# Performance work log

Measured on AMD Instinct MI355X. Metric: run time of the kernel, lower is better.

## Reference

```python
import jax, jax.numpy as jnp
import numpy as np

EPS = 1e-5

def conv3x3(x, w, b=None):
    # NCHW, OIHW, stride 1, padding 1
    y = jax.lax.conv_general_dilated(x, w, (1, 1), ((1, 1), (1, 1)),
                                     dimension_numbers=('NCHW', 'OIHW', 'NCHW'))
    if b is not None:
        y = y + b[None, :, None, None]
    return y

def batchnorm(x, g, b):
    # training-mode BN (PyTorch default): biased variance over (N,H,W)
    m = x.mean((0, 2, 3), keepdims=True)
    v = x.var((0, 2, 3), keepdims=True)
    return (x - m) * jax.lax.rsqrt(v + EPS) * g[None, :, None, None] + b[None, :, None, None]

def upsample2x_align_corners(x):
    # bilinear, align_corners=True, scale_factor=2
    def lerp_axis(a, Lin, axis):
        Lout = 2 * Lin
        c = jnp.arange(Lout, dtype=a.dtype) * (Lin - 1) / (Lout - 1)
        i0 = jnp.floor(c).astype(jnp.int32)
        i1 = jnp.minimum(i0 + 1, Lin - 1)
        w = c - i0.astype(a.dtype)
        shape = [1] * a.ndim
        shape[axis] = Lout
        w = w.reshape(shape)
        return jnp.take(a, i0, axis=axis) * (1 - w) + jnp.take(a, i1, axis=axis) * w
    x = lerp_axis(x, x.shape[2], 2)
    x = lerp_axis(x, x.shape[3], 3)
    return x

def deform_sample(x, offsets):
    # torchvision DeformConv2d v1 sampling: kernel 3x3, pad 1, offsets [B,18,H,W]
    # layout: per kernel point k (row-major), channels (2k, 2k+1) = (dy, dx)
    B, C, H, W = x.shape
    K = 9
    off = offsets.reshape(B, K, 2, H, W)
    ky, kx = jnp.meshgrid(jnp.arange(3) - 1, jnp.arange(3) - 1, indexing='ij')
    ky = ky.reshape(K).astype(x.dtype)
    kx = kx.reshape(K).astype(x.dtype)
    gy = jnp.arange(H, dtype=x.dtype)[None, None, :, None]
    gx = jnp.arange(W, dtype=x.dtype)[None, None, None, :]
    py = gy + ky[None, :, None, None] + off[:, :, 0]  # [B,K,H,W]
    px = gx + kx[None, :, None, None] + off[:, :, 1]
    y0 = jnp.floor(py)
    x0 = jnp.floor(px)
    wy = (py - y0)[:, None]  # [B,1,K,H,W]
    wx = (px - x0)[:, None]
    y0i = y0.astype(jnp.int32)
    x0i = x0.astype(jnp.int32)
    x_flat = x.reshape(B, C, H * W)
    def gather(yi, xi):
        valid = ((yi >= 0) & (yi < H) & (xi >= 0) & (xi < W))
        idx = jnp.clip(yi, 0, H - 1) * W + jnp.clip(xi, 0, W - 1)  # [B,K,H,W]
        g = jnp.take_along_axis(x_flat, idx.reshape(B, 1, K * H * W), axis=2)
        return g.reshape(B, C, K, H, W) * valid[:, None].astype(x.dtype)
    v00 = gather(y0i, x0i)
    v01 = gather(y0i, x0i + 1)
    v10 = gather(y0i + 1, x0i)
    v11 = gather(y0i + 1, x0i + 1)
    return (v00 * (1 - wy) * (1 - wx) + v01 * (1 - wy) * wx
            + v10 * wy * (1 - wx) + v11 * wy * wx)

def setup_inputs() -> dict:
    key = jax.random.key(0)
    ks = jax.random.split(key, 6)
    B, in_ch, skip_ch, out_ch = 4, 256, 128, 128
    Hs, Ws = 128, 128
    x = jax.random.normal(ks[0], (B, in_ch, Hs // 2, Ws // 2), jnp.float32)
    skip = jax.random.normal(ks[1], (B, skip_ch, Hs, Ws), jnp.float32)
    cat_ch = in_ch + skip_ch
    conv1_w = jax.random.normal(ks[2], (out_ch, cat_ch, 3, 3), jnp.float32) * (2.0 / (cat_ch * 9)) ** 0.5
    off_w = jax.random.normal(ks[3], (18, out_ch, 3, 3), jnp.float32) * 0.01
    off_b = jnp.zeros((18,), jnp.float32)
    def_w = jax.random.normal(ks[4], (out_ch, out_ch, 3, 3), jnp.float32) * (2.0 / (out_ch * 9)) ** 0.5
    def_b = jnp.zeros((out_ch,), jnp.float32)
    return {
        'x': x, 'skip': skip,
        'conv1_w': conv1_w,
        'bn1_g': jnp.ones((out_ch,), jnp.float32), 'bn1_b': jnp.zeros((out_ch,), jnp.float32),
        'off_w': off_w, 'off_b': off_b,
        'def_w': def_w, 'def_b': def_b,
        'bn2_g': jnp.ones((out_ch,), jnp.float32), 'bn2_b': jnp.zeros((out_ch,), jnp.float32),
    }

def reference(x, skip, conv1_w, bn1_g, bn1_b, off_w, off_b, def_w, def_b, bn2_g, bn2_b):
    xu = upsample2x_align_corners(x)
    dh = skip.shape[2] - xu.shape[2]
    dw = skip.shape[3] - xu.shape[3]
    if dh != 0 or dw != 0:
        xu = jnp.pad(xu, ((0, 0), (0, 0), (dh // 2, dh - dh // 2), (dw // 2, dw - dw // 2)))
    cat = jnp.concatenate([skip, xu], axis=1)
    h = jax.nn.relu(batchnorm(conv3x3(cat, conv1_w), bn1_g, bn1_b))
    offsets = conv3x3(h, off_w, off_b)  # [B,18,H,W]
    sampled = deform_sample(h, offsets)  # [B,C,9,H,W]
    O = def_w.shape[0]
    y = jnp.einsum('ock,bckhw->bohw', def_w.reshape(O, def_w.shape[1], 9), sampled)
    y = y + def_b[None, :, None, None]
    return jax.nn.relu(batchnorm(y, bn2_g, bn2_b))
```

## Files before the change

kernel.cpp:

```cpp
#include <hip/hip_runtime.h>
#include <hip/hip_bf16.h>

typedef __hip_bfloat16 bf16;
typedef __bf16 bf16x8 __attribute__((ext_vector_type(8)));
typedef __bf16 bf16x4 __attribute__((ext_vector_type(4)));
typedef float  f32x4  __attribute__((ext_vector_type(4)));

constexpr int NB   = 4;
constexpr int H    = 128;
constexpr int W    = 128;
constexpr int HW   = H * W;
constexpr int NPIX = NB * HW;
constexpr int CCAT = 384;
constexpr int CSKIP= 128;
constexpr int CIN  = 256;
constexpr int CO   = 128;
constexpr int HS   = 64;
constexpr int WP   = 130;
constexpr int K1   = 3456;
constexpr int KD   = 1152;
constexpr int NBORD= 2 * WP + 2 * (WP - 2);
constexpr float EPS = 1e-5f;

__device__ __forceinline__ float b2f(bf16 v){ return __bfloat162float(v); }
__device__ __forceinline__ bf16  f2b(float v){ return __float2bfloat16(v); }

__device__ __forceinline__ void async_copy16(const void* g, void* s){
    __builtin_amdgcn_global_load_lds((const __attribute__((address_space(1))) void*)g,
                                     (__attribute__((address_space(3))) void*)s, 16, 0, 0);
}

__device__ __forceinline__ void border_yx(int p, int& y, int& x){
    if (p < WP)             { y = 0;        x = p; }
    else if (p < 2 * WP)    { y = WP - 1;   x = p - WP; }
    else if (p < 2 * WP + (WP - 2)) { y = p - 2 * WP + 1;          x = 0; }
    else                    { y = p - (2 * WP + (WP - 2)) + 1;     x = WP - 1; }
}

__global__ void k_prep(float* __restrict__ sums, bf16* __restrict__ catp,
                       bf16* __restrict__ hp){
    int i = blockIdx.x * blockDim.x + threadIdx.x;
    int stride = gridDim.x * blockDim.x;
    for (int j = i; j < 512; j += stride) sums[j] = 0.f;
    const int nCat = NB * NBORD * CCAT;
    for (int j = i; j < nCat; j += stride){
        int c = j % CCAT, r = j / CCAT, p = r % NBORD, b = r / NBORD;
        int y, x; border_yx(p, y, x);
        catp[(((size_t)b * WP + y) * WP + x) * CCAT + c] = f2b(0.f);
    }
    const int nHp = NB * NBORD * CO;
    for (int j = i; j < nHp; j += stride){
        int c = j % CO, r = j / CO, p = r % NBORD, b = r / NBORD;
        int y, x; border_yx(p, y, x);
        hp[(((size_t)b * WP + y) * WP + x) * CO + c] = f2b(0.f);
    }
}

__global__ __launch_bounds__(256) void k_build_cat2(const float* __restrict__ x,
                                                    const float* __restrict__ skip,
                                                    bf16* __restrict__ catp){
    constexpr int TS = 66;
    __shared__ bf16 tile[128 * TS];
    int t  = threadIdx.x;
    int y  = blockIdx.x % H, b = blockIdx.x / H;
    int xx = t & 127, cp = t >> 7;

    float cy = (y * 63.0f) / 127.0f;
    int   y0 = (int)cy;
    int   y1 = min(y0 + 1, HS - 1);
    float wy = cy - y0;
    float cxf = (xx * 63.0f) / 127.0f;
    int   x0 = (int)cxf;
    int   x1 = min(x0 + 1, HS - 1);
    float wx = cxf - x0;

    bf16* orow = catp + (((size_t)b * WP + y + 1) * WP + 1) * CCAT;

    for (int chunk = 0; chunk < 6; chunk++){
        int cbase = chunk * 64;
        if (chunk >= 1) __syncthreads();
        if (chunk < 2){
            const float* sb = skip + ((size_t)(b * CSKIP + cbase + cp * 32) * H + y) * W;
#pragma unroll
            for (int i = 0; i < 32; i++)
                tile[xx * TS + cp * 32 + i] = f2b(sb[(size_t)i * HW + xx]);
        } else {
            int icb = (chunk - 2) * 64 + cp * 32;
            const float* xr0 = x + ((size_t)(b * CIN + icb) * HS + y0) * HS;
            const float* xr1 = x + ((size_t)(b * CIN + icb) * HS + y1) * HS;
#pragma unroll
            for (int i = 0; i < 32; i++){
                const float* r0 = xr0 + (size_t)i * HS * HS;
                const float* r1 = xr1 + (size_t)i * HS * HS;
                float v0 = r0[x0] * (1 - wx) + r0[x1] * wx;
                float v1 = r1[x0] * (1 - wx) + r1[x1] * wx;
                tile[xx * TS + cp * 32 + i] = f2b(v0 * (1 - wy) + v1 * wy);
            }
        }
        __syncthreads();
        int cc2 = (t & 31) * 2;
        int px0 = t >> 5;
#pragma unroll
        for (int pp = 0; pp < 16; pp++){
            int px = pp * 8 + px0;
            unsigned int v = *(const unsigned int*)&tile[px * TS + cc2];
            *(unsigned int*)&orow[(size_t)px * CCAT + cbase + cc2] = v;
        }
    }
}

__global__ void k_tr_all(const float* __restrict__ w1, const float* __restrict__ wo,
                         const float* __restrict__ wd,
                         bf16* __restrict__ wt1, bf16* __restrict__ wto,
                         bf16* __restrict__ wtd){
    int i = blockIdx.x * blockDim.x + threadIdx.x;
    if (i < CO * K1){
        int k = i % K1, oc = i / K1;
        int ky = k / 1152, r = k % 1152, kx = r / 384, ic = r % 384;
        wt1[i] = f2b(w1[((oc * CCAT + ic) * 3 + ky) * 3 + kx]);
        return;
    }
    i -= CO * K1;
    if (i < 32 * KD){
        int kk = i % KD, o = i / KD;
        int ky = kk / 384, r = kk % 384, kx = r >> 7, ic = r & 127;
        wto[i] = (o < 18) ? f2b(wo[((o * CO + ic) * 3 + ky) * 3 + kx]) : f2b(0.f);
        return;
    }
    i -= 32 * KD;
    if (i < CO * KD){
        int kk = i % KD, o = i / KD;
        int kp = kk >> 7, c = kk & 127;
        wtd[i] = f2b(wd[(o * CO + c) * 9 + kp]);
    }
}

__global__ __launch_bounds__(256) void k_conv1_mfma(const bf16* __restrict__ catp,
                                                    const bf16* __restrict__ wbt,
                                                    bf16* __restrict__ hp,
                                                    float* __restrict__ sums){
    __shared__ unsigned short Ab[132 * 128];
    __shared__ unsigned short Bb[128 * 64];
    __shared__ float ps[256];
    int t = threadIdx.x;
    int l = t & 63, w = t >> 6;
    int y = blockIdx.x % H, b = blockIdx.x / H;

    int pr   = l >> 3;
    int koct = (l & 7) ^ pr;
    int m    = l & 15, quad = l >> 4;
    int wm   = w & 1,  wn   = w >> 1;

    f32x4 acc[4][4];
#pragma unroll
    for (int i = 0; i < 4; i++)
#pragma unroll
        for (int j = 0; j < 4; j++) acc[i][j] = f32x4{0.f, 0.f, 0.f, 0.f};

    const size_t rowStride = (size_t)WP * CCAT;
    for (int ky = 0; ky < 3; ky++){
        const bf16* Arow = catp + ((size_t)(b * WP) + y + ky) * rowStride;
        for (int ci = 0; ci < 3; ci++){
            __syncthreads();
            for (int i = w; i < 33; i += 4){
                int G  = i * 64 + l;
                int px = G >> 4, ol = G & 15;
                int osrc = ol ^ (px & 7);
                async_copy16(Arow + (size_t)px * CCAT + ci * 128 + osrc * 8,
                             &Ab[i * 512]);
            }
            for (int kx = 0; kx < 3; kx++){
                for (int s64 = 0; s64 < 2; s64++){
                    if (kx | s64) __syncthreads();
                    int kg = ky * 1152 + kx * 384 + ci * 128 + s64 * 64;
#pragma unroll
                    for (int i = 0; i < 4; i++){
                        int ocg = w * 32 + i * 8;
                        async_copy16(wbt + (size_t)(ocg + pr) * K1 + kg + koct * 8,
                                     &Bb[ocg * 64]);
                    }
                    __syncthreads();
                    const bf16x8* ap = (const bf16x8*)Ab;
                    const bf16x8* bp = (const bf16x8*)Bb;
#pragma unroll
                    for (int ks = 0; ks < 2; ks++){
                        int s = s64 * 2 + ks;
                        bf16x8 af[4], bfr[4];
#pragma unroll
                        for (int mi = 0; mi < 4; mi++){
                            int pxk = wm * 64 + mi * 16 + m + kx;
                            af[mi] = ap[pxk * 16 + ((s * 4 + quad) ^ (pxk & 7))];
                        }
#pragma unroll
                        for (int ni = 0; ni < 4; ni++){
                            int oc = wn * 64 + ni * 16 + m;
                            bfr[ni] = bp[oc * 8 + ((ks * 4 + quad) ^ (oc & 7))];
                        }
#pragma unroll
                        for (int mi = 0; mi < 4; mi++)
#pragma unroll
                            for (int ni = 0; ni < 4; ni++)
                                acc[mi][ni] = __builtin_amdgcn_mfma_f32_16x16x32_bf16(
                                    af[mi], bfr[ni], acc[mi][ni], 0, 0, 0);
                    }
                }
            }
        }
    }
    size_t obase = (((size_t)b * WP + y + 1) * WP + 1) * CO;
#pragma unroll
    for (int mi = 0; mi < 4; mi++){
        int p0 = wm * 64 + mi * 16 + quad * 4;
#pragma unroll
        for (int ni = 0; ni < 4; ni++){
            int oc = wn * 64 + ni * 16 + m;
#pragma unroll
            for (int r = 0; r < 4; r++)
                hp[obase + (size_t)(p0 + r) * CO + oc] = f2b(acc[mi][ni][r]);
        }
    }
    ps[t] = 0.f;
    __syncthreads();
#pragma unroll
    for (int ni = 0; ni < 4; ni++){
        int ch = wn * 64 + ni * 16 + m;
        float s = 0.f, q = 0.f;
#pragma unroll
        for (int mi = 0; mi < 4; mi++)
#pragma unroll
            for (int r = 0; r < 4; r++){
                float v = acc[mi][ni][r];
                s += v; q += v * v;
            }
        s += __shfl_xor(s, 16); s += __shfl_xor(s, 32);
        q += __shfl_xor(q, 16); q += __shfl_xor(q, 32);
        if (quad == 0){
            atomicAdd(&ps[ch], s);
            atomicAdd(&ps[128 + ch], q);
        }
    }
    __syncthreads();
    if (t < 128){
        atomicAdd(&sums[t],       ps[t]);
        atomicAdd(&sums[128 + t], ps[128 + t]);
    }
}

__global__ __launch_bounds__(256) void k_bn_apply_pad(bf16* __restrict__ t,
                                                      const float* __restrict__ sums,
                                                      const float* __restrict__ g,
                                                      const float* __restrict__ bb){
    __shared__ float ssc[256];
    int tt = threadIdx.x;
    if (tt < 128){
        float mean = sums[tt] / (float)NPIX;
        float var  = sums[128 + tt] / (float)NPIX - mean * mean;
        float scale = g[tt] * rsqrtf(var + EPS);
        ssc[tt]       = scale;
        ssc[128 + tt] = bb[tt] - mean * scale;
    }
    __syncthreads();
    int i = blockIdx.x * 256 + tt;
    if (i >= NPIX * CO) return;
    int c = i & 127;
    int pix = i >> 7;
    int xw = pix & 127, yh = (pix >> 7) & 127, b = pix >> 14;
    size_t a = (((size_t)b * WP + yh + 1) * WP + xw + 1) * CO + c;
    float v = b2f(t[a]) * ssc[c] + ssc[128 + c];
    t[a] = f2b(v > 0.f ? v : 0.f);
}

__global__ __launch_bounds__(256) void k_conv_off_mfma(const bf16* __restrict__ hp,
                                                       const bf16* __restrict__ wob,
                                                       const float* __restrict__ off_b,
                                                       bf16* __restrict__ offs){
    __shared__ unsigned short Ab[132 * 128];
    __shared__ unsigned short Bb[32 * 384];
    int t = threadIdx.x, l = t & 63, w = t >> 6;
    int y = blockIdx.x % H, b = blockIdx.x / H;
    int m = l & 15, quad = l >> 4;
    int wm = w & 1, wn = w >> 1;

    f32x4 acc[4];
#pragma unroll
    for (int i = 0; i < 4; i++) acc[i] = f32x4{0.f, 0.f, 0.f, 0.f};

    const size_t rowStrideH = (size_t)WP * CO;
    for (int ky = 0; ky < 3; ky++){
        const bf16* Arow = hp + ((size_t)(b * WP) + y + ky) * rowStrideH;
        __syncthreads();
        for (int i = w; i < 33; i += 4){
            int G  = i * 64 + l;
            int px = G >> 4, ol = G & 15;
            int osrc = ol ^ (px & 7);
            async_copy16(Arow + (size_t)px * CO + osrc * 8, &Ab[i * 512]);
        }
        for (int i = w; i < 24; i += 4){
            int g  = i * 64 + l;
            int kx = g >> 9, oc = (g >> 4) & 31, ol = g & 15;
            int osrc = ol ^ (oc & 7);
            async_copy16(wob + (size_t)oc * KD + ky * 384 + kx * 128 + osrc * 8,
                         &Bb[i * 512]);
        }
        __syncthreads();
        const bf16x8* ap = (const bf16x8*)Ab;
        const bf16x8* bp = (const bf16x8*)Bb;
        for (int kx = 0; kx < 3; kx++){
#pragma unroll
            for (int s = 0; s < 4; s++){
                int oc = wn * 16 + m;
                bf16x8 bfr = bp[kx * 512 + oc * 16 + ((s * 4 + quad) ^ (oc & 7))];
#pragma unroll
                for (int mi = 0; mi < 4; mi++){
                    int pxk = wm * 64 + mi * 16 + m + kx;
                    bf16x8 af = ap[pxk * 16 + ((s * 4 + quad) ^ (pxk & 7))];
                    acc[mi] = __builtin_amdgcn_mfma_f32_16x16x32_bf16(af, bfr, acc[mi], 0, 0, 0);
                }
            }
        }
    }
    int oc = wn * 16 + m;
    if (oc < 18){
        float bias = off_b[oc];
        int rowpix = b * HW + y * W;
#pragma unroll
        for (int mi = 0; mi < 4; mi++){
            int p0 = wm * 64 + mi * 16 + quad * 4;
#pragma unroll
            for (int r = 0; r < 4; r++)
                offs[(size_t)(rowpix + p0 + r) * 18 + oc] = f2b(acc[mi][r] + bias);
        }
    }
}

__global__ __launch_bounds__(256) void k_deform_mfma(const bf16* __restrict__ hp,
                                                     const bf16* __restrict__ offs,
                                                     const bf16* __restrict__ wdb,
                                                     const float* __restrict__ def_b,
                                                     bf16* __restrict__ y,
                                                     float* __restrict__ sums){
    __shared__ unsigned short Ab[128 * 64];
    __shared__ unsigned short Bb[128 * 64];
    __shared__ int2   sc_yx[9 * 128];
    __shared__ float4 sc_w[9 * 128];
    __shared__ float  ps[256];

    int t = threadIdx.x, l = t & 63, w = t >> 6;
    int yrow = blockIdx.x % H, b = blockIdx.x / H;
    int rowpix = b * HW + yrow * W;

    for (int idx = t; idx < 9 * 128; idx += 256){
        int kp = idx >> 7, px = idx & 127;
        float dy = b2f(offs[(size_t)(rowpix + px) * 18 + 2 * kp]);
        float dx = b2f(offs[(size_t)(rowpix + px) * 18 + 2 * kp + 1]);
        float py = yrow + (kp / 3 - 1) + dy;
        float pxx = px + (kp % 3 - 1) + dx;
        float fy = floorf(py), fx = floorf(pxx);
        float wy = py - fy, wx = pxx - fx;
        int y0 = (int)fy, x0 = (int)fx;
        bool vy0 = (y0 >= 0) && (y0 < H);
        bool vy1 = (y0 + 1 >= 0) && (y0 + 1 < H);
        bool vx0 = (x0 >= 0) && (x0 < W);
        bool vx1 = (x0 + 1 >= 0) && (x0 + 1 < W);
        int y0c = min(max(y0, 0), H - 1),     y1c = min(max(y0 + 1, 0), H - 1);
        int x0c = min(max(x0, 0), W - 1),     x1c = min(max(x0 + 1, 0), W - 1);
        sc_yx[idx] = make_int2(((y0c + 1) * WP) | (((y1c + 1) * WP) << 16),
                               (x0c + 1) | ((x1c + 1) << 16));
        sc_w[idx] = make_float4((1 - wy) * (1 - wx) * (float)(vy0 && vx0),
                                (1 - wy) * wx       * (float)(vy0 && vx1),
                                wy * (1 - wx)       * (float)(vy1 && vx0),
                                wy * wx             * (float)(vy1 && vx1));
    }
    __syncthreads();

    int pr = l >> 3, koct = (l & 7) ^ pr;
    int m = l & 15, quad = l >> 4;
    int wm = w & 1, wn = w >> 1;
    int g = l >> 4, j = l & 15;

    f32x4 acc[4][4];
#pragma unroll
    for (int i = 0; i < 4; i++)
#pragma unroll
        for (int jj = 0; jj < 4; jj++) acc[i][jj] = f32x4{0.f, 0.f, 0.f, 0.f};

    const bf16* hpb = hp + (size_t)b * WP * WP * CO;

    for (int kc = 0; kc < 18; kc++){
        int kp = kc >> 1, ch = (kc & 1) * 64;
        __syncthreads();
        int kg = kp * 128 + ch;
#pragma unroll
        for (int i = 0; i < 4; i++){
            int oc = w * 32 + i * 8 + pr;
            async_copy16(wdb + (size_t)oc * KD + kg + koct * 8,
                         &Bb[(w * 32 + i * 8) * 64]);
        }
        int cb = ch + j * 4;
#pragma unroll
        for (int p = 0; p < 8; p++){
            int px = w * 32 + g * 8 + p;
            int idx = kp * 128 + px;
            int2 yx = sc_yx[idx];
            float4 w4 = sc_w[idx];
            int r0 = yx.x & 0xffff, r1 = ((unsigned)yx.x) >> 16;
            int c0 = yx.y & 0xffff, c1 = ((unsigned)yx.y) >> 16;
            const bf16* base = hpb + cb;
            bf16x4 s00 = *(const bf16x4*)(base + (size_t)(r0 + c0) * CO);
            bf16x4 s01 = *(const bf16x4*)(base + (size_t)(r0 + c1) * CO);
            bf16x4 s10 = *(const bf16x4*)(base + (size_t)(r1 + c0) * CO);
            bf16x4 s11 = *(const bf16x4*)(base + (size_t)(r1 + c1) * CO);
            bf16x4 pv;
#pragma unroll
            for (int r = 0; r < 4; r++){
                float v = w4.x * (float)s00[r] + w4.y * (float)s01[r]
                        + w4.z * (float)s10[r] + w4.w * (float)s11[r];
                pv[r] = (__bf16)v;
            }
            int oct_sw = (j >> 1) ^ (px & 7);
            *(bf16x4*)&Ab[px * 64 + oct_sw * 8 + (j & 1) * 4] = pv;
        }
        __syncthreads();
        const bf16x8* ap = (const bf16x8*)Ab;
        const bf16x8* bp = (const bf16x8*)Bb;
#pragma unroll
        for (int ks = 0; ks < 2; ks++){
            bf16x8 af[4], bfr[4];
#pragma unroll
            for (int mi = 0; mi < 4; mi++){
                int px = wm * 64 + mi * 16 + m;
                af[mi] = ap[px * 8 + ((ks * 4 + quad) ^ (px & 7))];
            }
#pragma unroll
            for (int ni = 0; ni < 4; ni++){
                int oc = wn * 64 + ni * 16 + m;
                bfr[ni] = bp[oc * 8 + ((ks * 4 + quad) ^ (oc & 7))];
            }
#pragma unroll
            for (int mi = 0; mi < 4; mi++)
#pragma unroll
                for (int ni = 0; ni < 4; ni++)
                    acc[mi][ni] = __builtin_amdgcn_mfma_f32_16x16x32_bf16(
                        af[mi], bfr[ni], acc[mi][ni], 0, 0, 0);
        }
    }
#pragma unroll
    for (int mi = 0; mi < 4; mi++){
        int p0 = wm * 64 + mi * 16 + quad * 4;
#pragma unroll
        for (int ni = 0; ni < 4; ni++){
            int oc = wn * 64 + ni * 16 + m;
            float bias = def_b[oc];
#pragma unroll
            for (int r = 0; r < 4; r++)
                y[(size_t)(rowpix + p0 + r) * CO + oc] = f2b(acc[mi][ni][r] + bias);
        }
    }
    ps[t] = 0.f;
    __syncthreads();
#pragma unroll
    for (int ni = 0; ni < 4; ni++){
        int ch = wn * 64 + ni * 16 + m;
        float bias = def_b[ch];
        float s = 0.f, q = 0.f;
#pragma unroll
        for (int mi = 0; mi < 4; mi++)
#pragma unroll
            for (int r = 0; r < 4; r++){
                float v = acc[mi][ni][r] + bias;
                s += v; q += v * v;
            }
        s += __shfl_xor(s, 16); s += __shfl_xor(s, 32);
        q += __shfl_xor(q, 16); q += __shfl_xor(q, 32);
        if (quad == 0){
            atomicAdd(&ps[ch], s);
            atomicAdd(&ps[128 + ch], q);
        }
    }
    __syncthreads();
    if (t < 128){
        atomicAdd(&sums[t],       ps[t]);
        atomicAdd(&sums[128 + t], ps[128 + t]);
    }
}

__global__ __launch_bounds__(256) void k_final(const bf16* __restrict__ yb,
                                               const float* __restrict__ sums,
                                               const float* __restrict__ g,
                                               const float* __restrict__ bb,
                                               float* __restrict__ out){
    __shared__ unsigned short tile[128 * 129];
    __shared__ float ssc[256];
    int t = threadIdx.x;
    if (t < 128){
        float mean = sums[t] / (float)NPIX;
        float var  = sums[128 + t] / (float)NPIX - mean * mean;
        float scale = g[t] * rsqrtf(var + EPS);
        ssc[t]       = scale;
        ssc[128 + t] = bb[t] - mean * scale;
    }
    int yrow = blockIdx.x % H, b = blockIdx.x / H;
    int rowbase = b * HW + yrow * W;
    const unsigned short* src = (const unsigned short*)yb;
    for (int it = 0; it < 64; it++){
        int idx = it * 256 + t;
        int c = idx & 127, px = idx >> 7;
        tile[px * 129 + c] = src[(size_t)(rowbase + px) * CO + c];
    }
    __syncthreads();
    for (int it = 0; it < 64; it++){
        int idx = it * 256 + t;
        int xw = idx & 127, o = idx >> 7;
        unsigned short u = tile[xw * 129 + o];
        float v = (float)(*(const __bf16*)&u);
        v = v * ssc[o] + ssc[128 + o];
        out[(((size_t)b * CO + o) * H + yrow) * W + xw] = v > 0.f ? v : 0.f;
    }
}

extern "C" void kernel_launch(void* const* d_in, const int* in_sizes, int n_in,
                              void* d_out, int out_size, void* d_ws, size_t ws_size,
                              hipStream_t stream){
    const float* x      = (const float*)d_in[0];
    const float* skip   = (const float*)d_in[1];
    const float* conv1w = (const float*)d_in[2];
    const float* bn1g   = (const float*)d_in[3];
    const float* bn1b   = (const float*)d_in[4];
    const float* offw   = (const float*)d_in[5];
    const float* offb   = (const float*)d_in[6];
    const float* defw   = (const float*)d_in[7];
    const float* defb   = (const float*)d_in[8];
    const float* bn2g   = (const float*)d_in[9];
    const float* bn2b   = (const float*)d_in[10];
    float* out = (float*)d_out;

    char* ws = (char*)d_ws;
    size_t off_bytes = 0;
    auto alloc = [&](size_t bytes) -> void* {
        void* p = ws + off_bytes;
        off_bytes += (bytes + 255) & ~(size_t)255;
        return p;
    };
    const size_t catp_elems = (size_t)NB * WP * WP * CCAT;
    const size_t hp_elems   = (size_t)NB * WP * WP * CO;
    bf16*  catp  = (bf16*) alloc(catp_elems * 2);
    bf16*  hp    = (bf16*) alloc(hp_elems * 2);
    bf16*  offs  = (bf16*) alloc((size_t)NPIX * 18 * 2);
    bf16*  yb    = (bf16*) alloc((size_t)NPIX * CO * 2);
    bf16*  wbt   = (bf16*) alloc((size_t)CO * K1 * 2);
    bf16*  wob   = (bf16*) alloc((size_t)32 * KD * 2);
    bf16*  wdb   = (bf16*) alloc((size_t)CO * KD * 2);
    float* sums  = (float*)alloc(512 * 4);
    float* sums1 = sums;
    float* sums2 = sums + 256;

    k_prep<<<1024, 256, 0, stream>>>(sums, catp, hp);

    k_build_cat2<<<NB * H, 256, 0, stream>>>(x, skip, catp);

    const int ntr = CO * K1 + 32 * KD + CO * KD;
    k_tr_all<<<(ntr + 255) / 256, 256, 0, stream>>>(conv1w, offw, defw, wbt, wob, wdb);

    k_conv1_mfma<<<NB * H, 256, 0, stream>>>(catp, wbt, hp, sums1);

    k_bn_apply_pad<<<(NPIX * CO + 255) / 256, 256, 0, stream>>>(hp, sums1, bn1g, bn1b);

    k_conv_off_mfma<<<NB * H, 256, 0, stream>>>(hp, wob, offb, offs);

    k_deform_mfma<<<NB * H, 256, 0, stream>>>(hp, offs, wdb, defb, yb, sums2);

    k_final<<<NB * H, 256, 0, stream>>>(yb, sums2, bn2g, bn2b, out);
}
```

Baseline: 334.6 us.

## Fuse offset conv into deformable conv kernel and merge weight prep kernels

Result: slower. 361.4 us (+8.0%).

```diff
diff --git a/kernel.cpp b/kernel.cpp
--- a/kernel.cpp
+++ b/kernel.cpp
@@ -37,22 +37,47 @@
     else                    { y = p - (2 * WP + (WP - 2)) + 1;     x = WP - 1; }
 }
 
-__global__ void k_prep(float* __restrict__ sums, bf16* __restrict__ catp,
-                       bf16* __restrict__ hp){
-    int i = blockIdx.x * blockDim.x + threadIdx.x;
+__global__ void k_prep_tr(float* __restrict__ sums, bf16* __restrict__ catp,
+                          bf16* __restrict__ hp,
+                          const float* __restrict__ w1, const float* __restrict__ wo,
+                          const float* __restrict__ wd,
+                          bf16* __restrict__ wt1, bf16* __restrict__ wto,
+                          bf16* __restrict__ wtd){
+    int i0 = blockIdx.x * blockDim.x + threadIdx.x;
     int stride = gridDim.x * blockDim.x;
-    for (int j = i; j < 512; j += stride) sums[j] = 0.f;
+    for (int j = i0; j < 512; j += stride) sums[j] = 0.f;
     const int nCat = NB * NBORD * CCAT;
-    for (int j = i; j < nCat; j += stride){
+    for (int j = i0; j < nCat; j += stride){
         int c = j % CCAT, r = j / CCAT, p = r % NBORD, b = r / NBORD;
         int y, x; border_yx(p, y, x);
         catp[(((size_t)b * WP + y) * WP + x) * CCAT + c] = f2b(0.f);
     }
     const int nHp = NB * NBORD * CO;
-    for (int j = i; j < nHp; j += stride){
+    for (int j = i0; j < nHp; j += stride){
         int c = j % CO, r = j / CO, p = r % NBORD, b = r / NBORD;
         int y, x; border_yx(p, y, x);
         hp[(((size_t)b * WP + y) * WP + x) * CO + c] = f2b(0.f);
+    }
+    const int ntr = CO * K1 + 32 * KD + CO * KD;
+    for (int j = i0; j < ntr; j += stride){
+        int i = j;
+        if (i < CO * K1){
+            int k = i % K1, oc = i / K1;
+            int ky = k / 1152, r = k % 1152, kx = r / 384, ic = r % 384;
+            wt1[i] = f2b(w1[((oc * CCAT + ic) * 3 + ky) * 3 + kx]);
+            continue;
+        }
+        i -= CO * K1;
+        if (i < 32 * KD){
+            int kk = i % KD, o = i / KD;
+            int ky = kk / 384, r = kk % 384, kx = r >> 7, ic = r & 127;
+            wto[i] = (o < 18) ? f2b(wo[((o * CO + ic) * 3 + ky) * 3 + kx]) : f2b(0.f);
+            continue;
+        }
+        i -= 32 * KD;
+        int kk = i % KD, o = i / KD;
+        int kp = kk >> 7, c = kk & 127;
+        wtd[i] = f2b(wd[(o * CO + c) * 9 + kp]);
     }
 }
 
@@ -106,32 +131,6 @@
             unsigned int v = *(const unsigned int*)&tile[px * TS + cc2];
             *(unsigned int*)&orow[(size_t)px * CCAT + cbase + cc2] = v;
         }
-    }
-}
-
-__global__ void k_tr_all(const float* __restrict__ w1, const float* __restrict__ wo,
-                         const float* __restrict__ wd,
-                         bf16* __restrict__ wt1, bf16* __restrict__ wto,
-                         bf16* __restrict__ wtd){
-    int i = blockIdx.x * blockDim.x + threadIdx.x;
-    if (i < CO * K1){
-        int k = i % K1, oc = i / K1;
-        int ky = k / 1152, r = k % 1152, kx = r / 384, ic = r % 384;
-        wt1[i] = f2b(w1[((oc * CCAT + ic) * 3 + ky) * 3 + kx]);
-        return;
-    }
-    i -= CO * K1;
-    if (i < 32 * KD){
-        int kk = i % KD, o = i / KD;
-        int ky = kk / 384, r = kk % 384, kx = r >> 7, ic = r & 127;
-        wto[i] = (o < 18) ? f2b(wo[((o * CO + ic) * 3 + ky) * 3 + kx]) : f2b(0.f);
-        return;
-    }
-    i -= 32 * KD;
-    if (i < CO * KD){
-        int kk = i % KD, o = i / KD;
-        int kp = kk >> 7, c = kk & 127;
-        wtd[i] = f2b(wd[(o * CO + c) * 9 + kp]);
     }
 }
 
@@ -270,41 +269,54 @@
     t[a] = f2b(v > 0.f ? v : 0.f);
 }
 
-__global__ __launch_bounds__(256) void k_conv_off_mfma(const bf16* __restrict__ hp,
-                                                       const bf16* __restrict__ wob,
-                                                       const float* __restrict__ off_b,
-                                                       bf16* __restrict__ offs){
-    __shared__ unsigned short Ab[132 * 128];
-    __shared__ unsigned short Bb[32 * 384];
+__global__ __launch_bounds__(256) void k_offdef_mfma(const bf16* __restrict__ hp,
+                                                     const bf16* __restrict__ wob,
+                                                     const float* __restrict__ off_b,
+                                                     const bf16* __restrict__ wdb,
+                                                     const float* __restrict__ def_b,
+                                                     bf16* __restrict__ y,
+                                                     float* __restrict__ sums){
+    __shared__ __align__(16) char smem[71680];
+    unsigned short* AbBig = (unsigned short*)smem;
+    unsigned short* BbOff = (unsigned short*)(smem + 33792);
+    unsigned short* dAb   = (unsigned short*)smem;
+    unsigned short* dBb   = (unsigned short*)(smem + 16384);
+    int2*   sc_yx = (int2*)(smem + 33792);
+    float4* sc_w  = (float4*)(smem + 43008);
+    float*  offst = (float*)(smem + 61440);
+    float*  ps    = (float*)(smem + 70656);
+
     int t = threadIdx.x, l = t & 63, w = t >> 6;
-    int y = blockIdx.x % H, b = blockIdx.x / H;
+    int yrow = blockIdx.x % H, b = blockIdx.x / H;
+    int rowpix = b * HW + yrow * W;
     int m = l & 15, quad = l >> 4;
     int wm = w & 1, wn = w >> 1;
-
-    f32x4 acc[4];
-#pragma unroll
-    for (int i = 0; i < 4; i++) acc[i] = f32x4{0.f, 0.f, 0.f, 0.f};
+    int pr = l >> 3, koct = (l & 7) ^ pr;
+
+    f32x4 aoff[4];
+#pragma unroll
+    for (int i = 0; i < 4; i++) aoff[i] = f32x4{0.f, 0.f, 0.f, 0.f};
 
     const size_t rowStrideH = (size_t)WP * CO;
     for (int ky = 0; ky < 3; ky++){
-        const bf16* Arow = hp + ((size_t)(b * WP) + y + ky) * rowStrideH;
+        const bf16* Arow = hp + ((size_t)(b * WP) + yrow + ky) * rowStrideH;
         __syncthreads();
         for (int i = w; i < 33; i += 4){
             int G  = i * 64 + l;
             int px = G >> 4, ol = G & 15;
             int osrc = ol ^ (px & 7);
-            async_copy16(Arow + (size_t)px * CO + osrc * 8, &Ab[i * 512]);
+            async_copy16(Arow + (size_t)px * CO + osrc * 8, &AbBig[i * 512]);
         }
         for (int i = w; i < 24; i += 4){
-            int g  = i * 64 + l;
-            int kx = g >> 9, oc = (g >> 4) & 31, ol = g & 15;
+            int gg = i * 64 + l;
+            int kx = gg >> 9, oc = (gg >> 4) & 31, ol = gg & 15;
             int osrc = ol ^ (oc & 7);
             async_copy16(wob + (size_t)oc * KD + ky * 384 + kx * 128 + osrc * 8,
-                         &Bb[i * 512]);
+                         &BbOff[i * 512]);
         }
         __syncthreads();
-        const bf16x8* ap = (const bf16x8*)Ab;
-        const bf16x8* bp = (const bf16x8*)Bb;
+        const bf16x8* ap = (const bf16x8*)AbBig;
+        const bf16x8* bp = (const bf16x8*)BbOff;
         for (int kx = 0; kx < 3; kx++){
 #pragma unroll
             for (int s = 0; s < 4; s++){
@@ -314,45 +326,30 @@
                 for (int mi = 0; mi < 4; mi++){
                     int pxk = wm * 64 + mi * 16 + m + kx;
                     bf16x8 af = ap[pxk * 16 + ((s * 4 + quad) ^ (pxk & 7))];
-                    acc[mi] = __builtin_amdgcn_mfma_f32_16x16x32_bf16(af, bfr, acc[mi], 0, 0, 0);
+                    aoff[mi] = __builtin_amdgcn_mfma_f32_16x16x32_bf16(af, bfr, aoff[mi], 0, 0, 0);
                 }
             }
         }
     }
-    int oc = wn * 16 + m;
-    if (oc < 18){
-        float bias = off_b[oc];
-        int rowpix = b * HW + y * W;
-#pragma unroll
-        for (int mi = 0; mi < 4; mi++){
-            int p0 = wm * 64 + mi * 16 + quad * 4;
-#pragma unroll
-            for (int r = 0; r < 4; r++)
-                offs[(size_t)(rowpix + p0 + r) * 18 + oc] = f2b(acc[mi][r] + bias);
-        }
-    }
-}
-
-__global__ __launch_bounds__(256) void k_deform_mfma(const bf16* __restrict__ hp,
-                                                     const bf16* __restrict__ offs,
-                                                     const bf16* __restrict__ wdb,
-                                                     const float* __restrict__ def_b,
-                                                     bf16* __restrict__ y,
-                                                     float* __restrict__ sums){
-    __shared__ unsigned short Ab[128 * 64];
-    __shared__ unsigned short Bb[128 * 64];
-    __shared__ int2   sc_yx[9 * 128];
-    __shared__ float4 sc_w[9 * 128];
-    __shared__ float  ps[256];
-
-    int t = threadIdx.x, l = t & 63, w = t >> 6;
-    int yrow = blockIdx.x % H, b = blockIdx.x / H;
-    int rowpix = b * HW + yrow * W;
+    {
+        int oc = wn * 16 + m;
+        if (oc < 18){
+            float bias = off_b[oc];
+#pragma unroll
+            for (int mi = 0; mi < 4; mi++){
+                int p0 = wm * 64 + mi * 16 + quad * 4;
+#pragma unroll
+                for (int r = 0; r < 4; r++)
+                    offst[(p0 + r) * 18 + oc] = aoff[mi][r] + bias;
+            }
+        }
+    }
+    __syncthreads();
 
     for (int idx = t; idx < 9 * 128; idx += 256){
         int kp = idx >> 7, px = idx & 127;
-        float dy = b2f(offs[(size_t)(rowpix + px) * 18 + 2 * kp]);
-        float dx = b2f(offs[(size_t)(rowpix + px) * 18 + 2 * kp + 1]);
+        float dy = offst[px * 18 + 2 * kp];
+        float dx = offst[px * 18 + 2 * kp + 1];
         float py = yrow + (kp / 3 - 1) + dy;
         float pxx = px + (kp % 3 - 1) + dx;
         float fy = floorf(py), fx = floorf(pxx);
@@ -373,10 +370,7 @@
     }
     __syncthreads();
 
-    int pr = l >> 3, koct = (l & 7) ^ pr;
-    int m = l & 15, quad = l >> 4;
-    int wm = w & 1, wn = w >> 1;
-    int g = l >> 4, j = l & 15;
+    int gg = l >> 4, j = l & 15;
 
     f32x4 acc[4][4];
 #pragma unroll
@@ -394,12 +388,12 @@
         for (int i = 0; i < 4; i++){
             int oc = w * 32 + i * 8 + pr;
             async_copy16(wdb + (size_t)oc * KD + kg + koct * 8,
-                         &Bb[(w * 32 + i * 8) * 64]);
+                         &dBb[(w * 32 + i * 8) * 64]);
         }
         int cb = ch + j * 4;
 #pragma unroll
         for (int p = 0; p < 8; p++){
-            int px = w * 32 + g * 8 + p;
+            int px = w * 32 + gg * 8 + p;
             int idx = kp * 128 + px;
             int2 yx = sc_yx[idx];
             float4 w4 = sc_w[idx];
@@ -418,11 +412,11 @@
                 pv[r] = (__bf16)v;
             }
             int oct_sw = (j >> 1) ^ (px & 7);
-            *(bf16x4*)&Ab[px * 64 + oct_sw * 8 + (j & 1) * 4] = pv;
+            *(bf16x4*)&dAb[px * 64 + oct_sw * 8 + (j & 1) * 4] = pv;
         }
         __syncthreads();
-        const bf16x8* ap = (const bf16x8*)Ab;
-        const bf16x8* bp = (const bf16x8*)Bb;
+        const bf16x8* ap = (const bf16x8*)dAb;
+        const bf16x8* bp = (const bf16x8*)dBb;
 #pragma unroll
         for (int ks = 0; ks < 2; ks++){
             bf16x8 af[4], bfr[4];
@@ -545,7 +539,6 @@
     const size_t hp_elems   = (size_t)NB * WP * WP * CO;
     bf16*  catp  = (bf16*) alloc(catp_elems * 2);
     bf16*  hp    = (bf16*) alloc(hp_elems * 2);
-    bf16*  offs  = (bf16*) alloc((size_t)NPIX * 18 * 2);
     bf16*  yb    = (bf16*) alloc((size_t)NPIX * CO * 2);
     bf16*  wbt   = (bf16*) alloc((size_t)CO * K1 * 2);
     bf16*  wob   = (bf16*) alloc((size_t)32 * KD * 2);
@@ -554,20 +547,16 @@
     float* sums1 = sums;
     float* sums2 = sums + 256;
 
-    k_prep<<<1024, 256, 0, stream>>>(sums, catp, hp);
+    k_prep_tr<<<2048, 256, 0, stream>>>(sums, catp, hp, conv1w, offw, defw,
+                                        wbt, wob, wdb);
 
     k_build_cat2<<<NB * H, 256, 0, stream>>>(x, skip, catp);
 
-    const int ntr = CO * K1 + 32 * KD + CO * KD;
-    k_tr_all<<<(ntr + 255) / 256, 256, 0, stream>>>(conv1w, offw, defw, wbt, wob, wdb);
-
     k_conv1_mfma<<<NB * H, 256, 0, stream>>>(catp, wbt, hp, sums1);
 
     k_bn_apply_pad<<<(NPIX * CO + 255) / 256, 256, 0, stream>>>(hp, sums1, bn1g, bn1b);
 
-    k_conv_off_mfma<<<NB * H, 256, 0, stream>>>(hp, wob, offb, offs);
-
-    k_deform_mfma<<<NB * H, 256, 0, stream>>>(hp, offs, wdb, defb, yb, sums2);
+    k_offdef_mfma<<<NB * H, 256, 0, stream>>>(hp, wob, offb, wdb, defb, yb, sums2);
 
     k_final<<<NB * H, 256, 0, stream>>>(yb, sums2, bn2g, bn2b, out);
 }
```
